# Kernel tuning notes

Measured on AMD Instinct MI355X. Metric: run time of the kernel, lower is better.

The kernel has to match this reference:

```python
import jax, jax.numpy as jnp
import numpy as np

N, C_IN, H, W = 8, 512, 56, 56
CH = 128  # make_divisible(512*0.25, 8)
SCALE = CH ** (-0.5)
BN_EPS = 1e-5


def setup_inputs() -> dict:
    key = jax.random.key(0)
    ks = jax.random.split(key, 6)
    x = jax.random.normal(ks[0], (N, C_IN, H, W), dtype=jnp.float32)
    # 1x1 conv W: in_channels -> 3*channels (with bias)
    W_w = jax.random.normal(ks[1], (3 * CH, C_IN), dtype=jnp.float32) * (2.0 / C_IN) ** 0.5
    W_b = jnp.zeros((3 * CH,), dtype=jnp.float32)
    # 1x1 conv Z: channels -> in_channels (no bias, followed by BN)
    Z_w = jax.random.normal(ks[2], (C_IN, CH), dtype=jnp.float32) * (2.0 / CH) ** 0.5
    bn_gamma = jax.random.normal(ks[3], (C_IN,), dtype=jnp.float32) * 0.1
    bn_beta = jnp.zeros((C_IN,), dtype=jnp.float32)
    bn_mean = jnp.zeros((C_IN,), dtype=jnp.float32)
    bn_var = jnp.ones((C_IN,), dtype=jnp.float32)
    return {"x": x, "W_w": W_w, "W_b": W_b, "Z_w": Z_w,
            "bn_gamma": bn_gamma, "bn_beta": bn_beta,
            "bn_mean": bn_mean, "bn_var": bn_var}


def reference(x, W_w, W_b, Z_w, bn_gamma, bn_beta, bn_mean, bn_var):
    n, c, h, w = x.shape
    xf = x.reshape(n, c, h * w)                               # [N, C, HW]
    proj = jnp.einsum('oc,ncq->noq', W_w, xf) + W_b[None, :, None]  # [N, 3*CH, HW]
    t, p, g = jnp.split(proj, 3, axis=1)                      # each [N, CH, HW]
    s = jnp.einsum('ncq,nck->nqk', t, p)                      # [N, HW, HW]
    s = jax.nn.softmax(s * SCALE, axis=2)
    att = jnp.einsum('nqv,ncv->ncq', s, g)                    # [N, CH, HW]
    z = jnp.einsum('oc,ncq->noq', Z_w, att)                   # [N, C, HW]
    # BatchNorm2d, inference form with running stats
    inv = bn_gamma / jnp.sqrt(bn_var + BN_EPS)
    z = z * inv[None, :, None] + (bn_beta - bn_mean * inv)[None, :, None]
    return z.reshape(n, c, h, w) + x
```

## Files before the change

### kernel.cpp

```cpp
#include <hip/hip_runtime.h>
#include <hip/hip_bf16.h>
#include <math.h>

#define NB    8
#define CIN   512
#define HW    3136
#define CH    128
#define TCH   384
#define SCALE 0.08838834764831845f
#define QKSCALE 0.12751744f
#define BNEPS 1e-5f
#define NSPLIT 5
#define QB    128

typedef __attribute__((ext_vector_type(8)))  short bf16x8;
typedef __attribute__((ext_vector_type(4)))  short bf16x4;
typedef __attribute__((ext_vector_type(4)))  float f32x4;
typedef __attribute__((ext_vector_type(16))) float f32x16;

#define MFMA16(a, b, c) __builtin_amdgcn_mfma_f32_16x16x32_bf16((a), (b), (c), 0, 0, 0)
#define MFMA32(a, b, c) __builtin_amdgcn_mfma_f32_32x32x16_bf16((a), (b), (c), 0, 0, 0)

__device__ inline short f2bf(float f) {
    __hip_bfloat16 h = __float2bfloat16(f);
    return *reinterpret_cast<short*>(&h);
}
__device__ inline unsigned pack2bf(float a, float b) {
    return (unsigned)(unsigned short)f2bf(a) | ((unsigned)(unsigned short)f2bf(b) << 16);
}
__device__ inline unsigned cvtpk(float lo, float hi) {
    unsigned r;
    asm("v_cvt_pk_bf16_f32 %0, %1, %2" : "=v"(r) : "v"(lo), "v"(hi));
    return r;
}
__device__ inline float bfraw2f(unsigned short u) {
    return __uint_as_float(((unsigned)u) << 16);
}
__device__ inline float exp2a(float x) {
    float r; asm("v_exp_f32 %0, %1" : "=v"(r) : "v"(x)); return r;
}

__global__ __launch_bounds__(256) void cvt_wts(const float* __restrict__ Ww,
                                               const float* __restrict__ Zw,
                                               __hip_bfloat16* __restrict__ WwB,
                                               __hip_bfloat16* __restrict__ ZwB) {
    const int nW = TCH * CIN / 4;
    const int nZ = CIN * CH / 4;
    int i = blockIdx.x * 256 + threadIdx.x;
    if (i < nW) {
        float4 v = ((const float4*)Ww)[i];
        bf16x4 o; o[0] = f2bf(v.x); o[1] = f2bf(v.y); o[2] = f2bf(v.z); o[3] = f2bf(v.w);
        ((bf16x4*)WwB)[i] = o;
    } else if (i < nW + nZ) {
        int j = i - nW;
        float4 v = ((const float4*)Zw)[j];
        bf16x4 o; o[0] = f2bf(v.x); o[1] = f2bf(v.y); o[2] = f2bf(v.z); o[3] = f2bf(v.w);
        ((bf16x4*)ZwB)[j] = o;
    }
}

__global__ __launch_bounds__(256) void xpose_kernel(const float* __restrict__ x,
                                                    __hip_bfloat16* __restrict__ xT) {
    const int n = blockIdx.z, c0 = blockIdx.y * 64, q0 = blockIdx.x * 64;
    const int tid = threadIdx.x;
    const int mr = tid >> 4, mq = tid & 15;

    __shared__ char T[64 * 128];

    const float* xp = x + ((size_t)(n * CIN + c0 + mr * 4)) * HW + q0 + mq * 4;
    float4 r0 = *(const float4*)(xp);
    float4 r1 = *(const float4*)(xp + HW);
    float4 r2 = *(const float4*)(xp + 2 * HW);
    float4 r3 = *(const float4*)(xp + 3 * HW);
    const float* f0 = (const float*)&r0; const float* f1 = (const float*)&r1;
    const float* f2 = (const float*)&r2; const float* f3 = (const float*)&r3;
#pragma unroll
    for (int j = 0; j < 4; ++j) {
        int q = mq * 4 + j;
        bf16x4 v; v[0] = f2bf(f0[j]); v[1] = f2bf(f1[j]);
                  v[2] = f2bf(f2[j]); v[3] = f2bf(f3[j]);
        *(bf16x4*)(T + q * 128 + ((mr * 8) ^ ((q & 15) << 3))) = v;
    }
    __syncthreads();

    __hip_bfloat16* og = xT + ((size_t)n * HW + q0) * CIN + c0;
#pragma unroll
    for (int it = 0; it < 2; ++it) {
        int ch = it * 256 + tid, rr = ch >> 3, o8 = ch & 7;
        int sw = (rr & 15) << 3;
        bf16x4 lo = *(const bf16x4*)(T + rr * 128 + ((o8 * 16) ^ sw));
        bf16x4 hi = *(const bf16x4*)(T + rr * 128 + ((o8 * 16 + 8) ^ sw));
        bf16x8 v; v[0] = lo[0]; v[1] = lo[1]; v[2] = lo[2]; v[3] = lo[3];
                  v[4] = hi[0]; v[5] = hi[1]; v[6] = hi[2]; v[7] = hi[3];
        *(bf16x8*)(og + (size_t)rr * CIN + o8 * 8) = v;
    }
}

__global__ __launch_bounds__(256) void proj_kernel(const __hip_bfloat16* __restrict__ xT,
                                                   const __hip_bfloat16* __restrict__ WwB,
                                                   const float* __restrict__ Wb,
                                                   __hip_bfloat16* __restrict__ Qt,
                                                   __hip_bfloat16* __restrict__ Kt,
                                                   __hip_bfloat16* __restrict__ Vg) {
    const int q0 = blockIdx.x * 64;
    if (q0 >= HW) return;
    const int n  = blockIdx.z;
    const int m0 = blockIdx.y * 64;
    const int tid = threadIdx.x;
    const int lane = tid & 63, wv = tid >> 6;
    const int lr = lane & 15, hi = lane >> 4;

    __shared__ char Aw[64 * 128];
    __shared__ char Bx[64 * 128];
    __shared__ char Ts[64 * 128];

    f32x4 acc[4] = {};
    const __hip_bfloat16* xn = xT + ((size_t)n * HW + q0) * CIN;

    for (int k0 = 0; k0 < CIN; k0 += 64) {
#pragma unroll
        for (int it = 0; it < 2; ++it) {
            int ch = it * 256 + tid, r = ch >> 3, o = ch & 7;
            int sw = (o * 16) ^ ((r & 7) << 4);
            bf16x8 a = *(const bf16x8*)(WwB + (size_t)(m0 + r) * CIN + k0 + o * 8);
            *(bf16x8*)(Aw + r * 128 + sw) = a;
            bf16x8 b = *(const bf16x8*)(xn + (size_t)r * CIN + k0 + o * 8);
            *(bf16x8*)(Bx + r * 128 + sw) = b;
        }
        __syncthreads();

        const int mrow = wv * 16 + lr;
#pragma unroll
        for (int ks = 0; ks < 2; ++ks) {
            bf16x8 af = *(const bf16x8*)(Aw + mrow * 128 +
                                         ((ks * 64 + hi * 16) ^ ((mrow & 7) << 4)));
#pragma unroll
            for (int kn = 0; kn < 4; ++kn) {
                int qrow = kn * 16 + lr;
                bf16x8 bfr = *(const bf16x8*)(Bx + qrow * 128 +
                                              ((ks * 64 + hi * 16) ^ ((qrow & 7) << 4)));
                acc[kn] = MFMA16(af, bfr, acc[kn]);
            }
        }
        __syncthreads();
    }

    const int region = m0 >> 7;
    const int c0     = m0 & 127;
    const float oscale = (region == 0) ? QKSCALE : 1.0f;

    float bias[4];
#pragma unroll
    for (int reg = 0; reg < 4; ++reg) bias[reg] = Wb[m0 + wv * 16 + hi * 4 + reg];

#pragma unroll
    for (int kn = 0; kn < 4; ++kn)
#pragma unroll
        for (int reg = 0; reg < 4; ++reg) {
            __hip_bfloat16 v = __float2bfloat16((acc[kn][reg] + bias[reg]) * oscale);
            int row, colb;
            if (region < 2) { row = kn * 16 + lr; colb = (wv * 16 + hi * 4 + reg) * 2; }
            else            { row = wv * 16 + hi * 4 + reg; colb = (kn * 16 + lr) * 2; }
            *(__hip_bfloat16*)(Ts + row * 128 + (colb ^ ((row & 7) << 4))) = v;
        }
    __syncthreads();

    __hip_bfloat16* base;
    size_t rstride;
    if (region == 0)      { base = Qt + (size_t)n * HW * CH + (size_t)q0 * CH + c0; rstride = CH; }
    else if (region == 1) { base = Kt + (size_t)n * HW * CH + (size_t)q0 * CH + c0; rstride = CH; }
    else                  { base = Vg + (size_t)n * CH * HW + (size_t)c0 * HW + q0; rstride = HW; }

#pragma unroll
    for (int it = 0; it < 2; ++it) {
        int ch = it * 256 + tid, rr = ch >> 3, o = ch & 7;
        bf16x8 v = *(const bf16x8*)(Ts + rr * 128 + ((o * 16) ^ ((rr & 7) << 4)));
        *(bf16x8*)(base + (size_t)rr * rstride + o * 8) = v;
    }
}

__global__ __launch_bounds__(256, 2) void attn_kernel(
        const __hip_bfloat16* __restrict__ Qt,
        const __hip_bfloat16* __restrict__ Kt,
        const __hip_bfloat16* __restrict__ Vg,
        __hip_bfloat16* __restrict__ PO0,
        __hip_bfloat16* __restrict__ PO4,
        float* __restrict__ Mbuf,
        float* __restrict__ Lbuf) {
    const int n = blockIdx.x & 7, s = blockIdx.x >> 3;
    const int q0 = blockIdx.y * QB;
    const int tid = threadIdx.x;
    const int lane = tid & 63, wv = tid >> 6;
    const int l31 = lane & 31, h = lane >> 5;

    __shared__ char smem[32768];
    char* Ks = smem;
    char* Vt = smem + 16384;

    const int t0 = s * 10;
    const int t1 = (s == 4) ? 49 : (t0 + 10);

    const __hip_bfloat16* Kg = Kt + (size_t)n * HW * CH;
    const __hip_bfloat16* Vp = Vg + (size_t)n * CH * HW;

    const int qg = q0 + wv * 32 + l31;
    const int qc = (qg < HW) ? qg : (HW - 1);
    const __hip_bfloat16* Qg = Qt + ((size_t)n * HW + qc) * CH + h * 8;
    bf16x8 qf[8];
#pragma unroll
    for (int cs = 0; cs < 8; ++cs) qf[cs] = *(const bf16x8*)(Qg + cs * 16);

    const int kr = tid >> 2, kgb = (tid & 3) * 4;
    const int ksz = (kr & 7) ^ (((kr >> 3) & 1) << 3);
    const int vr = tid >> 1, vgb = (tid & 1) * 4;
    const int vsz = vr & 7;
    const __hip_bfloat16* Ksrc = Kg + (size_t)kr * CH;
    const __hip_bfloat16* Vsrc = Vp + (size_t)vr * HW;
    char* Kd = Ks + kr * 256;
    char* Vd = Vt + vr * 128;

    bf16x8 kreg[4], vreg[4];
    {
        const int kk = t0 * 64;
#pragma unroll
        for (int i = 0; i < 4; ++i)
            kreg[i] = *(const bf16x8*)(Ksrc + (size_t)kk * CH + (kgb + i) * 8);
#pragma unroll
        for (int i = 0; i < 4; ++i)
            vreg[i] = *(const bf16x8*)(Vsrc + kk + (vgb + i) * 8);
    }
#pragma unroll
    for (int i = 0; i < 4; ++i) *(bf16x8*)(Kd + ((kgb + i) ^ ksz) * 16) = kreg[i];
#pragma unroll
    for (int i = 0; i < 4; ++i) *(bf16x8*)(Vd + ((vgb + i) ^ vsz) * 16) = vreg[i];
    __syncthreads();

    const int rsw = (l31 & 7) ^ (((l31 >> 3) & 1) << 3);
    const int vrsw = l31 & 7;

    f32x16 O[4] = {};
    float m_i = -1e30f, l_i = 0.f;

    for (int t = t0; t < t1; ++t) {
        if (t + 1 < t1) {
            const int kk = (t + 1) * 64;
#pragma unroll
            for (int i = 0; i < 4; ++i)
                kreg[i] = *(const bf16x8*)(Ksrc + (size_t)kk * CH + (kgb + i) * 8);
#pragma unroll
            for (int i = 0; i < 4; ++i)
                vreg[i] = *(const bf16x8*)(Vsrc + kk + (vgb + i) * 8);
        }

        f32x16 sa0 = {}, sa1 = {};
        __builtin_amdgcn_s_setprio(1);
#pragma unroll
        for (int cs = 0; cs < 8; ++cs) {
            int goff = ((cs * 2 + h) ^ rsw) * 16;
            bf16x8 k0f = *(const bf16x8*)(Ks + l31 * 256 + goff);
            bf16x8 k1f = *(const bf16x8*)(Ks + (32 + l31) * 256 + goff);
            sa0 = MFMA32(k0f, qf[cs], sa0);
            sa1 = MFMA32(k1f, qf[cs], sa1);
        }
        __builtin_amdgcn_s_setprio(0);

        float tm[16];
#pragma unroll
        for (int r = 0; r < 16; ++r) tm[r] = fmaxf(sa0[r], sa1[r]);
#pragma unroll
        for (int st = 8; st >= 1; st >>= 1)
#pragma unroll
            for (int r = 0; r < st; ++r) tm[r] = fmaxf(tm[r], tm[r + st]);
        float pmax = tm[0];
        pmax = fmaxf(pmax, __shfl_xor(pmax, 32));

        if (__any(pmax > m_i + 8.0f)) {
            float nm = fmaxf(m_i, pmax);
            float f  = exp2a(m_i - nm);
            l_i *= f; m_i = nm;
#pragma unroll
            for (int ct = 0; ct < 4; ++ct)
#pragma unroll
                for (int r = 0; r < 16; ++r) O[ct][r] *= f;
        }

#pragma unroll
        for (int r = 0; r < 16; ++r) sa0[r] = exp2a(sa0[r] - m_i);
#pragma unroll
        for (int r = 0; r < 16; ++r) sa1[r] = exp2a(sa1[r] - m_i);
        float ts[16];
#pragma unroll
        for (int r = 0; r < 16; ++r) ts[r] = sa0[r] + sa1[r];
#pragma unroll
        for (int st = 8; st >= 1; st >>= 1)
#pragma unroll
            for (int r = 0; r < st; ++r) ts[r] += ts[r + st];
        float rs = ts[0];
        rs += __shfl_xor(rs, 32);
        l_i += rs;

        union { unsigned u[4]; bf16x8 v; } pf0, pf1, pf2, pf3;
        {
            unsigned w0 = cvtpk(sa0[0],  sa0[1]),  w1 = cvtpk(sa0[2],  sa0[3]);
            unsigned w2 = cvtpk(sa0[4],  sa0[5]),  w3 = cvtpk(sa0[6],  sa0[7]);
            unsigned w4 = cvtpk(sa0[8],  sa0[9]),  w5 = cvtpk(sa0[10], sa0[11]);
            unsigned w6 = cvtpk(sa0[12], sa0[13]), w7 = cvtpk(sa0[14], sa0[15]);
            asm("v_permlane32_swap_b32 %0, %1" : "+v"(w0), "+v"(w2));
            asm("v_permlane32_swap_b32 %0, %1" : "+v"(w1), "+v"(w3));
            asm("v_permlane32_swap_b32 %0, %1" : "+v"(w4), "+v"(w6));
            asm("v_permlane32_swap_b32 %0, %1" : "+v"(w5), "+v"(w7));
            pf0.u[0] = w0; pf0.u[1] = w1; pf0.u[2] = w2; pf0.u[3] = w3;
            pf1.u[0] = w4; pf1.u[1] = w5; pf1.u[2] = w6; pf1.u[3] = w7;
        }
        {
            unsigned w0 = cvtpk(sa1[0],  sa1[1]),  w1 = cvtpk(sa1[2],  sa1[3]);
            unsigned w2 = cvtpk(sa1[4],  sa1[5]),  w3 = cvtpk(sa1[6],  sa1[7]);
            unsigned w4 = cvtpk(sa1[8],  sa1[9]),  w5 = cvtpk(sa1[10], sa1[11]);
            unsigned w6 = cvtpk(sa1[12], sa1[13]), w7 = cvtpk(sa1[14], sa1[15]);
            asm("v_permlane32_swap_b32 %0, %1" : "+v"(w0), "+v"(w2));
            asm("v_permlane32_swap_b32 %0, %1" : "+v"(w1), "+v"(w3));
            asm("v_permlane32_swap_b32 %0, %1" : "+v"(w4), "+v"(w6));
            asm("v_permlane32_swap_b32 %0, %1" : "+v"(w5), "+v"(w7));
            pf2.u[0] = w0; pf2.u[1] = w1; pf2.u[2] = w2; pf2.u[3] = w3;
            pf3.u[0] = w4; pf3.u[1] = w5; pf3.u[2] = w6; pf3.u[3] = w7;
        }

        __builtin_amdgcn_s_setprio(1);
#pragma unroll
        for (int ct = 0; ct < 4; ++ct) {
            const char* vrow = Vt + (ct * 32 + l31) * 128;
            bf16x8 v0 = *(const bf16x8*)(vrow + ((0 + h) ^ vrsw) * 16);
            bf16x8 v1 = *(const bf16x8*)(vrow + ((2 + h) ^ vrsw) * 16);
            bf16x8 v2 = *(const bf16x8*)(vrow + ((4 + h) ^ vrsw) * 16);
            bf16x8 v3 = *(const bf16x8*)(vrow + ((6 + h) ^ vrsw) * 16);
            O[ct] = MFMA32(v0, pf0.v, O[ct]);
            O[ct] = MFMA32(v1, pf1.v, O[ct]);
            O[ct] = MFMA32(v2, pf2.v, O[ct]);
            O[ct] = MFMA32(v3, pf3.v, O[ct]);
        }
        __builtin_amdgcn_s_setprio(0);

        __syncthreads();
        if (t + 1 < t1) {
#pragma unroll
            for (int i = 0; i < 4; ++i) *(bf16x8*)(Kd + ((kgb + i) ^ ksz) * 16) = kreg[i];
#pragma unroll
            for (int i = 0; i < 4; ++i) *(bf16x8*)(Vd + ((vgb + i) ^ vsz) * 16) = vreg[i];
        }
        __syncthreads();
    }

    const int qrow = wv * 32 + l31;
    const int esw  = (qrow & 7) << 4;
#pragma unroll
    for (int ct = 0; ct < 4; ++ct)
#pragma unroll
        for (int i = 0; i < 8; ++i) {
            int c = ct * 32 + 2 * (i & 1) + 8 * (i >> 1) + 4 * h;
            unsigned u = pack2bf(O[ct][2 * i], O[ct][2 * i + 1]);
            *(unsigned*)(smem + qrow * 256 + ((c * 2) ^ esw)) = u;
        }
    __syncthreads();
    __hip_bfloat16* pbase = (s < 4) ? (PO0 + (size_t)s * NB * HW * CH) : PO4;
    __hip_bfloat16* pg = pbase + ((size_t)n * HW + q0) * CH;
#pragma unroll
    for (int it = 0; it < 8; ++it) {
        int ch = it * 256 + tid, r = ch >> 4, g = ch & 15;
        if (q0 + r < HW) {
            bf16x8 v = *(const bf16x8*)(smem + r * 256 + ((g * 16) ^ ((r & 7) << 4)));
            *(bf16x8*)(pg + (size_t)r * CH + g * 8) = v;
        }
    }
    if (h == 0 && qg < HW) {
        size_t base = (size_t)(s * NB + n) * HW + qg;
        Mbuf[base] = m_i; Lbuf[base] = l_i;
    }
}

__global__ __launch_bounds__(256) void merge_kernel(
        const __hip_bfloat16* __restrict__ PO0,
        const __hip_bfloat16* __restrict__ PO4,
        const float* __restrict__ Mbuf,
        const float* __restrict__ Lbuf,
        __hip_bfloat16* __restrict__ att) {
    const int idx = blockIdx.x * 256 + threadIdx.x;
    const int nq = idx >> 4;
    const int c0 = (idx & 15) * 8;
    const size_t NHW = (size_t)NB * HW;

    float m[NSPLIT], l[NSPLIT];
#pragma unroll
    for (int s = 0; s < NSPLIT; ++s) { m[s] = Mbuf[s * NHW + nq]; l[s] = Lbuf[s * NHW + nq]; }
    float M = m[0];
#pragma unroll
    for (int s = 1; s < NSPLIT; ++s) M = fmaxf(M, m[s]);
    float w[NSPLIT], denom = 0.f;
#pragma unroll
    for (int s = 0; s < NSPLIT; ++s) { w[s] = exp2f(m[s] - M); denom += w[s] * l[s]; }
    float rinv = 1.f / denom;

    float acc[8] = {};
#pragma unroll
    for (int s = 0; s < NSPLIT; ++s) {
        const __hip_bfloat16* pbase = (s < 4) ? (PO0 + (size_t)s * NHW * CH) : PO4;
        union { bf16x8 v; unsigned short u[8]; } p;
        p.v = *(const bf16x8*)(pbase + (size_t)nq * CH + c0);
#pragma unroll
        for (int j = 0; j < 8; ++j) acc[j] += w[s] * bfraw2f(p.u[j]);
    }
    union { bf16x8 v; unsigned short u[8]; } ov;
#pragma unroll
    for (int j = 0; j < 8; ++j) ov.u[j] = (unsigned short)f2bf(acc[j] * rinv);
    *(bf16x8*)(att + (size_t)nq * CH + c0) = ov.v;
}

__global__ __launch_bounds__(256) void zbn_kernel(const __hip_bfloat16* __restrict__ att,
                                                  const __hip_bfloat16* __restrict__ ZwB,
                                                  const float* __restrict__ gamma,
                                                  const float* __restrict__ beta,
                                                  const float* __restrict__ mean,
                                                  const float* __restrict__ var,
                                                  const float* __restrict__ x,
                                                  float* __restrict__ out) {
    const int q0 = blockIdx.x * 64;
    if (q0 >= HW) return;
    const int n  = blockIdx.z;
    const int m0 = blockIdx.y * 64;
    const int tid = threadIdx.x;
    const int lane = tid & 63, wv = tid >> 6;
    const int lr = lane & 15, hi = lane >> 4;

    __shared__ char smem[32768];
    char* Az = smem;
    char* Ba = smem + 16384;

#pragma unroll
    for (int it = 0; it < 4; ++it) {
        int ch = it * 256 + tid, r = ch >> 4, o = ch & 15;
        int sw = (o * 16) ^ ((r & 7) << 4);
        bf16x8 a = *(const bf16x8*)(ZwB + (size_t)(m0 + r) * CH + o * 8);
        *(bf16x8*)(Az + r * 256 + sw) = a;
        bf16x8 b = *(const bf16x8*)(att + ((size_t)n * HW + q0 + r) * CH + o * 8);
        *(bf16x8*)(Ba + r * 256 + sw) = b;
    }
    __syncthreads();

    f32x4 acc[4] = {};
    const int mrow = wv * 16 + lr;
#pragma unroll
    for (int ks = 0; ks < 4; ++ks) {
        bf16x8 af = *(const bf16x8*)(Az + mrow * 256 +
                                     ((ks * 64 + hi * 16) ^ ((mrow & 7) << 4)));
#pragma unroll
        for (int kn = 0; kn < 4; ++kn) {
            int qrow = kn * 16 + lr;
            bf16x8 bfr = *(const bf16x8*)(Ba + qrow * 256 +
                                          ((ks * 64 + hi * 16) ^ ((qrow & 7) << 4)));
            acc[kn] = MFMA16(af, bfr, acc[kn]);
        }
    }
    __syncthreads();

    float inv[4], add[4];
#pragma unroll
    for (int reg = 0; reg < 4; ++reg) {
        int m = m0 + wv * 16 + hi * 4 + reg;
        inv[reg] = gamma[m] * rsqrtf(var[m] + BNEPS);
        add[reg] = beta[m] - mean[m] * inv[reg];
    }

#pragma unroll
    for (int kn = 0; kn < 4; ++kn)
#pragma unroll
        for (int reg = 0; reg < 4; ++reg) {
            int row = wv * 16 + hi * 4 + reg;
            int colb = (kn * 16 + lr) * 4;
            *(float*)(smem + row * 256 + (colb ^ ((row & 7) << 4))) =
                acc[kn][reg] * inv[reg] + add[reg];
        }
    __syncthreads();

#pragma unroll
    for (int it = 0; it < 4; ++it) {
        int ch = it * 256 + tid, rr = ch >> 4, o = ch & 15;
        f32x4 v = *(const f32x4*)(smem + rr * 256 + ((o * 16) ^ ((rr & 7) << 4)));
        size_t idx = (size_t)n * CIN * HW + (size_t)(m0 + rr) * HW + q0 + o * 4;
        float4 xv = *(const float4*)(x + idx);
        float4 ov; ov.x = v[0] + xv.x; ov.y = v[1] + xv.y;
                   ov.z = v[2] + xv.z; ov.w = v[3] + xv.w;
        *(float4*)(out + idx) = ov;
    }
}

extern "C" void kernel_launch(void* const* d_in, const int* in_sizes, int n_in,
                              void* d_out, int out_size, void* d_ws, size_t ws_size,
                              hipStream_t stream) {
    const float* x     = (const float*)d_in[0];
    const float* Ww    = (const float*)d_in[1];
    const float* Wb    = (const float*)d_in[2];
    const float* Zw    = (const float*)d_in[3];
    const float* gamma = (const float*)d_in[4];
    const float* beta  = (const float*)d_in[5];
    const float* mean  = (const float*)d_in[6];
    const float* var   = (const float*)d_in[7];
    float* out = (float*)d_out;

    const size_t xT_bytes  = (size_t)NB * HW * CIN * 2;
    const size_t qkv_bytes = (size_t)NB * HW * CH * 2;
    char* ob = (char*)d_out;
    __hip_bfloat16* xT  = (__hip_bfloat16*)ob;
    __hip_bfloat16* Qt  = (__hip_bfloat16*)(ob + xT_bytes);
    __hip_bfloat16* Kt  = (__hip_bfloat16*)(ob + xT_bytes + qkv_bytes);
    __hip_bfloat16* Vgb = (__hip_bfloat16*)(ob + xT_bytes + 2 * qkv_bytes);
    __hip_bfloat16* PO0 = (__hip_bfloat16*)ob;
    __hip_bfloat16* PO4 = (__hip_bfloat16*)(ob + xT_bytes + 3 * qkv_bytes);

    char* w = (char*)d_ws;
    __hip_bfloat16* attb = (__hip_bfloat16*)w;                       w += qkv_bytes;
    __hip_bfloat16* WwB  = (__hip_bfloat16*)w;                       w += (size_t)TCH * CIN * 2;
    __hip_bfloat16* ZwB  = (__hip_bfloat16*)w;                       w += (size_t)CIN * CH * 2;
    float* Mbuf = (float*)w;                                         w += (size_t)NSPLIT * NB * HW * 4;
    float* Lbuf = (float*)w;

    cvt_wts<<<dim3(256), 256, 0, stream>>>(Ww, Zw, WwB, ZwB);
    xpose_kernel<<<dim3(HW / 64, CIN / 64, NB), 256, 0, stream>>>(x, xT);
    proj_kernel<<<dim3(56, TCH / 64, NB), 256, 0, stream>>>(xT, WwB, Wb, Qt, Kt, Vgb);
    attn_kernel<<<dim3(NB * NSPLIT, (HW + QB - 1) / QB), 256, 0, stream>>>(
        Qt, Kt, Vgb, PO0, PO4, Mbuf, Lbuf);
    merge_kernel<<<dim3(NB * HW * 16 / 256), 256, 0, stream>>>(PO0, PO4, Mbuf, Lbuf, attb);
    zbn_kernel<<<dim3(56, CIN / 64, NB), 256, 0, stream>>>(attb, ZwB, gamma, beta,
                                                           mean, var, x, out);
}
```

Measured before the change: 126.6 us.

## Double-buffer K/V tiles in LDS to drop one barrier per attention iteration

Shared memory grows to two K/V tile buffers that alternate between consecutive key tiles. Each iteration first stores the register-prefetched tile t+1 into the idle buffer, then issues the global loads for tile t+2, then computes on the current buffer. This removes the second __syncthreads per iteration and overlaps LDS stores with MFMA work. In exchange, LDS per block doubles to 64KB, which may limit how many blocks fit per CU, and the loop is unrolled by two.

```diff
diff --git a/kernel.cpp b/kernel.cpp
--- a/kernel.cpp
+++ b/kernel.cpp
@@ -193,9 +193,11 @@
     const int lane = tid & 63, wv = tid >> 6;
     const int l31 = lane & 31, h = lane >> 5;
 
-    __shared__ char smem[32768];
-    char* Ks = smem;
-    char* Vt = smem + 16384;
+    __shared__ char smem[65536];
+    char* KsA = smem;
+    char* VtA = smem + 16384;
+    char* KsB = smem + 32768;
+    char* VtB = smem + 49152;
 
     const int t0 = s * 10;
     const int t1 = (s == 4) ? 49 : (t0 + 10);
@@ -216,8 +218,8 @@
     const int vsz = vr & 7;
     const __hip_bfloat16* Ksrc = Kg + (size_t)kr * CH;
     const __hip_bfloat16* Vsrc = Vp + (size_t)vr * HW;
-    char* Kd = Ks + kr * 256;
-    char* Vd = Vt + vr * 128;
+    const int kdo = kr * 256;
+    const int vdo = vr * 128;
 
     bf16x8 kreg[4], vreg[4];
     {
@@ -230,10 +232,19 @@
             vreg[i] = *(const bf16x8*)(Vsrc + kk + (vgb + i) * 8);
     }
 #pragma unroll
-    for (int i = 0; i < 4; ++i) *(bf16x8*)(Kd + ((kgb + i) ^ ksz) * 16) = kreg[i];
-#pragma unroll
-    for (int i = 0; i < 4; ++i) *(bf16x8*)(Vd + ((vgb + i) ^ vsz) * 16) = vreg[i];
-    __syncthreads();
+    for (int i = 0; i < 4; ++i) *(bf16x8*)(KsA + kdo + ((kgb + i) ^ ksz) * 16) = kreg[i];
+#pragma unroll
+    for (int i = 0; i < 4; ++i) *(bf16x8*)(VtA + vdo + ((vgb + i) ^ vsz) * 16) = vreg[i];
+    __syncthreads();
+    if (t0 + 1 < t1) {
+        const int kk = (t0 + 1) * 64;
+#pragma unroll
+        for (int i = 0; i < 4; ++i)
+            kreg[i] = *(const bf16x8*)(Ksrc + (size_t)kk * CH + (kgb + i) * 8);
+#pragma unroll
+        for (int i = 0; i < 4; ++i)
+            vreg[i] = *(const bf16x8*)(Vsrc + kk + (vgb + i) * 8);
+    }
 
     const int rsw = (l31 & 7) ^ (((l31 >> 3) & 1) << 3);
     const int vrsw = l31 & 7;
@@ -241,9 +252,15 @@
     f32x16 O[4] = {};
     float m_i = -1e30f, l_i = 0.f;
 
-    for (int t = t0; t < t1; ++t) {
+    auto ITER = [&](int t, char* CK, char* CV, char* NK, char* NV) {
         if (t + 1 < t1) {
-            const int kk = (t + 1) * 64;
+#pragma unroll
+            for (int i = 0; i < 4; ++i) *(bf16x8*)(NK + kdo + ((kgb + i) ^ ksz) * 16) = kreg[i];
+#pragma unroll
+            for (int i = 0; i < 4; ++i) *(bf16x8*)(NV + vdo + ((vgb + i) ^ vsz) * 16) = vreg[i];
+        }
+        if (t + 2 < t1) {
+            const int kk = (t + 2) * 64;
 #pragma unroll
             for (int i = 0; i < 4; ++i)
                 kreg[i] = *(const bf16x8*)(Ksrc + (size_t)kk * CH + (kgb + i) * 8);
@@ -257,8 +274,8 @@
 #pragma unroll
         for (int cs = 0; cs < 8; ++cs) {
             int goff = ((cs * 2 + h) ^ rsw) * 16;
-            bf16x8 k0f = *(const bf16x8*)(Ks + l31 * 256 + goff);
-            bf16x8 k1f = *(const bf16x8*)(Ks + (32 + l31) * 256 + goff);
+            bf16x8 k0f = *(const bf16x8*)(CK + l31 * 256 + goff);
+            bf16x8 k1f = *(const bf16x8*)(CK + (32 + l31) * 256 + goff);
             sa0 = MFMA32(k0f, qf[cs], sa0);
             sa1 = MFMA32(k1f, qf[cs], sa1);
         }
@@ -328,7 +345,7 @@
         __builtin_amdgcn_s_setprio(1);
 #pragma unroll
         for (int ct = 0; ct < 4; ++ct) {
-            const char* vrow = Vt + (ct * 32 + l31) * 128;
+            const char* vrow = CV + (ct * 32 + l31) * 128;
             bf16x8 v0 = *(const bf16x8*)(vrow + ((0 + h) ^ vrsw) * 16);
             bf16x8 v1 = *(const bf16x8*)(vrow + ((2 + h) ^ vrsw) * 16);
             bf16x8 v2 = *(const bf16x8*)(vrow + ((4 + h) ^ vrsw) * 16);
@@ -341,13 +358,11 @@
         __builtin_amdgcn_s_setprio(0);
 
         __syncthreads();
-        if (t + 1 < t1) {
-#pragma unroll
-            for (int i = 0; i < 4; ++i) *(bf16x8*)(Kd + ((kgb + i) ^ ksz) * 16) = kreg[i];
-#pragma unroll
-            for (int i = 0; i < 4; ++i) *(bf16x8*)(Vd + ((vgb + i) ^ vsz) * 16) = vreg[i];
-        }
-        __syncthreads();
+    };
+
+    for (int t = t0; t < t1; t += 2) {
+        ITER(t, KsA, VtA, KsB, VtB);
+        if (t + 1 < t1) ITER(t + 1, KsB, VtB, KsA, VtA);
     }
 
     const int qrow = wv * 32 + l31;
```

Measured after the change: 127.5 us. About the same (+0.7%).
